# Kernel optimization log

Hardware: AMD Instinct MI355X
Metric: run time of the kernel (lower is better)

Reference implementation:

```python
import jax, jax.numpy as jnp
import numpy as np

N = 100000       # nodes
E = 1600000      # edges
V = 50000        # vocab
H = 256          # embedding dim (hsize)
A = 64           # per-head out dim (asize)
NH = 3           # num_heads
G = 64           # graphs in batch


def setup_inputs() -> dict:
    key = jax.random.key(0)
    ks = jax.random.split(key, 12)
    h0 = jax.random.randint(ks[0], (N,), 0, V)
    src = jax.random.randint(ks[1], (E,), 0, N)
    dst = jax.random.randint(ks[2], (E,), 0, N)
    graph_ids = jnp.sort(jax.random.randint(ks[3], (N,), 0, G))
    s = 0.05
    emb = jax.random.normal(ks[4], (V, H), jnp.float32) * s
    W_fc = jax.random.normal(ks[5], (H, NH * A), jnp.float32) * s   # GATConv fc
    attn_l = jax.random.normal(ks[6], (NH, A), jnp.float32) * s
    attn_r = jax.random.normal(ks[7], (NH, A), jnp.float32) * s
    bias_gat = jax.random.normal(ks[8], (NH, A), jnp.float32) * s
    W1 = jax.random.normal(ks[9], (A, 128), jnp.float32) * s
    b1 = jnp.zeros((128,), jnp.float32)
    W2 = jax.random.normal(ks[10], (128, 16), jnp.float32) * s
    b2 = jnp.zeros((16,), jnp.float32)
    return dict(h0=h0, src=src, dst=dst, graph_ids=graph_ids, emb=emb,
                W_fc=W_fc, attn_l=attn_l, attn_r=attn_r, bias_gat=bias_gat,
                W1=W1, b1=b1, W2=W2, b2=b2)


def reference(h0, src, dst, graph_ids, emb, W_fc, attn_l, attn_r, bias_gat,
              W1, b1, W2, b2):
    # embedding lookup
    h1 = emb[h0]                                            # [N, H]
    # GATConv: linear projection per head
    feat = (h1 @ W_fc).reshape(N, NH, A)                    # [N, NH, A]
    el = jnp.einsum('nha,ha->nh', feat, attn_l)             # [N, NH]
    er = jnp.einsum('nha,ha->nh', feat, attn_r)             # [N, NH]
    e = jax.nn.leaky_relu(el[src] + er[dst], 0.2)           # [E, NH]
    # segment softmax over incoming edges of each dst node
    m = jax.ops.segment_max(e, dst, num_segments=N)         # [N, NH]
    e_exp = jnp.exp(e - m[dst])                             # [E, NH]
    denom = jax.ops.segment_sum(e_exp, dst, num_segments=N) # [N, NH]
    alpha = e_exp / denom[dst]                              # [E, NH]
    # scatter-aggregate messages
    msg = alpha[:, :, None] * feat[src]                     # [E, NH, A]
    rst = jax.ops.segment_sum(msg, dst, num_segments=N)     # [N, NH, A]
    rst = rst + bias_gat[None]                              # GATConv bias
    # relu + mean over heads
    h2 = jnp.mean(jax.nn.relu(rst), axis=1)                 # [N, A]
    # MLP predictor: ReLU then Identity
    h3 = jax.nn.relu(h2 @ W1 + b1) @ W2 + b2                # [N, 16]
    # dgl.mean_nodes: per-graph mean readout
    sums = jax.ops.segment_sum(h3, graph_ids, num_segments=G)            # [G, 16]
    counts = jax.ops.segment_sum(jnp.ones((N,), h3.dtype), graph_ids, num_segments=G)
    return sums / jnp.maximum(counts, 1.0)[:, None]         # [G, 16]
```

## Files before the change

kernel.cpp:

```cpp
#include <hip/hip_runtime.h>
#include <hip/hip_bf16.h>

#define NNODES 100000
#define NEDGES 1600000
#define VOCAB 50000
#define HDIM 256
#define ADIM 64
#define NHEADS 3
#define FDIM 192
#define NGRAPH 64
#define NPART 64

#define CONV_ELEMS (HDIM * FDIM + 128 * 64 + 16 * 128)
#define CONV_BLOCKS ((CONV_ELEMS + 255) / 256)
#define HIST_BLOCKS ((NEDGES + 255) / 256)
#define PREP_BLOCKS 3
#define ELVR_BLOCKS ((VOCAB + 3) / 4)
#define PROJ_BLOCKS ((VOCAB + 63) / 64)
#define SCAT_BLOCKS ((NEDGES / 4 + 255) / 256)
#define NB ((NNODES + 1023) / 1024)

typedef __attribute__((ext_vector_type(8))) short bf16x8;
typedef __attribute__((ext_vector_type(4))) float f32x4;

__device__ __forceinline__ float bf2f(unsigned short u) {
  return __uint_as_float((unsigned int)u << 16);
}
__device__ __forceinline__ unsigned short f2bf(float f) {
  unsigned int u = __float_as_uint(f);
  u += 0x7FFFu + ((u >> 16) & 1u);
  return (unsigned short)(u >> 16);
}

__global__ __launch_bounds__(256) void conv_hist_prep_kernel(
    const float* __restrict__ Wfc, const float* __restrict__ W1,
    const float* __restrict__ W2, unsigned short* __restrict__ Wt,
    unsigned short* __restrict__ W1t, unsigned short* __restrict__ W2t,
    const int* __restrict__ src, const int* __restrict__ dst,
    const int* __restrict__ h0, int* __restrict__ cnt,
    unsigned short* __restrict__ rank16,
    unsigned short* __restrict__ vsrc16, unsigned short* __restrict__ vdst16,
    const float* __restrict__ al, const float* __restrict__ ar,
    float* __restrict__ wl, float* __restrict__ wr)
{
  if (blockIdx.x < CONV_BLOCKS) {
    int i = blockIdx.x * 256 + threadIdx.x;
    if (i < HDIM * FDIM) {
      int c = i / HDIM, k = i % HDIM;
      Wt[i] = f2bf(Wfc[(size_t)k * FDIM + c]);
    } else if (i < HDIM * FDIM + 128 * 64) {
      int j = i - HDIM * FDIM;
      int c = j / 64, k = j % 64;
      W1t[j] = f2bf(W1[(size_t)k * 128 + c]);
    } else if (i < CONV_ELEMS) {
      int j = i - HDIM * FDIM - 128 * 64;
      int c = j / 128, k = j % 128;
      W2t[j] = f2bf(W2[(size_t)k * 16 + c]);
    }
    return;
  }
  if (blockIdx.x < CONV_BLOCKS + HIST_BLOCKS) {
    int e = (blockIdx.x - CONV_BLOCKS) * 256 + threadIdx.x;
    if (e < NEDGES) {
      int s = src[e], d = dst[e];
      rank16[e]  = (unsigned short)atomicAdd(&cnt[d], 1);
      vsrc16[e]  = (unsigned short)h0[s];
      vdst16[e]  = (unsigned short)h0[d];
    }
    return;
  }
  int t = (blockIdx.x - CONV_BLOCKS - HIST_BLOCKS) * 256 + threadIdx.x;
  if (t >= 3 * 256) return;
  int h = t >> 8, k = t & 255;
  const float* a_l = &al[h * 64];
  const float* a_r = &ar[h * 64];
  const float* row = &Wfc[(size_t)k * FDIM + h * 64];
  float sl = 0.f, sr = 0.f;
#pragma unroll 16
  for (int c = 0; c < 64; ++c) {
    float w = row[c];
    sl += w * a_l[c];
    sr += w * a_r[c];
  }
  wl[h * 256 + k] = sl;
  wr[h * 256 + k] = sr;
}

__global__ __launch_bounds__(256) void scan_elvr_kernel(
    const int* __restrict__ cnt, int* __restrict__ offs,
    const float* __restrict__ emb, const float* __restrict__ wl,
    const float* __restrict__ wr, float4* __restrict__ elv4,
    float4* __restrict__ erv4)
{
  if (blockIdx.x < NB) {
    __shared__ int sd[256];
    __shared__ int base_sh;
    const int i = blockIdx.x, t = threadIdx.x;
    const int pre = i * 1024;
    int s = 0;
    for (int j = t * 4; j < pre; j += 1024) {
      int4 v = *reinterpret_cast<const int4*>(&cnt[j]);
      s += v.x + v.y + v.z + v.w;
    }
    sd[t] = s;
    __syncthreads();
    for (int o = 128; o > 0; o >>= 1) {
      if (t < o) sd[t] += sd[t + o];
      __syncthreads();
    }
    if (t == 0) base_sh = sd[0];
    __syncthreads();
    const int base = base_sh;
    __syncthreads();
    int bstart = pre + t * 4;
    int c[4];
    int ts = 0;
#pragma unroll
    for (int j = 0; j < 4; ++j) {
      c[j] = (bstart + j < NNODES) ? cnt[bstart + j] : 0;
      ts += c[j];
    }
    sd[t] = ts;
    __syncthreads();
    for (int o = 1; o < 256; o <<= 1) {
      int v = (t >= o) ? sd[t - o] : 0;
      __syncthreads();
      sd[t] += v;
      __syncthreads();
    }
    int run = sd[t] - ts + base;
#pragma unroll
    for (int j = 0; j < 4; ++j) {
      if (bstart + j < NNODES) offs[bstart + j] = run;
      run += c[j];
    }
    if (i == NB - 1 && t == 255) offs[NNODES] = base + sd[255];
    return;
  }
  int v = (blockIdx.x - NB) * 4 + (threadIdx.x >> 6);
  int lane = threadIdx.x & 63;
  if (v >= VOCAB) return;
  const float* er_ = &emb[(size_t)v * HDIM];
  float e0 = er_[lane], e1 = er_[64 + lane], e2 = er_[128 + lane], e3 = er_[192 + lane];
  float sl[3], sr[3];
#pragma unroll
  for (int h = 0; h < 3; ++h) {
    const float* wlh = &wl[h * 256];
    const float* wrh = &wr[h * 256];
    sl[h] = e0 * wlh[lane] + e1 * wlh[64 + lane] + e2 * wlh[128 + lane] + e3 * wlh[192 + lane];
    sr[h] = e0 * wrh[lane] + e1 * wrh[64 + lane] + e2 * wrh[128 + lane] + e3 * wrh[192 + lane];
  }
#pragma unroll
  for (int s = 32; s > 0; s >>= 1) {
#pragma unroll
    for (int h = 0; h < 3; ++h) {
      sl[h] += __shfl_xor(sl[h], s, 64);
      sr[h] += __shfl_xor(sr[h], s, 64);
    }
  }
  if (lane == 0) {
    elv4[v] = make_float4(sl[0], sl[1], sl[2], 0.f);
    erv4[v] = make_float4(sr[0], sr[1], sr[2], 0.f);
  }
}

__global__ __launch_bounds__(256) void proj_scatter_kernel(
    const float* __restrict__ emb,
    const unsigned short* __restrict__ Wt,
    unsigned short* __restrict__ proj_bf,
    const int* __restrict__ dst,
    const unsigned short* __restrict__ rank16,
    const unsigned short* __restrict__ vsrc16,
    const unsigned short* __restrict__ vdst16,
    const int* __restrict__ offs,
    const float4* __restrict__ elv4, const float4* __restrict__ erv4,
    uint2* __restrict__ wrec)
{
  if (blockIdx.x >= PROJ_BLOCKS) {
    int t = (blockIdx.x - PROJ_BLOCKS) * 256 + threadIdx.x;
    int e0 = t * 4;
    if (e0 >= NEDGES) return;
    int4    d4 = *reinterpret_cast<const int4*>(&dst[e0]);
    ushort4 r4 = *reinterpret_cast<const ushort4*>(&rank16[e0]);
    ushort4 s4 = *reinterpret_cast<const ushort4*>(&vsrc16[e0]);
    ushort4 v4 = *reinterpret_cast<const ushort4*>(&vdst16[e0]);
    int dd[4] = {d4.x, d4.y, d4.z, d4.w};
    int rr[4] = {r4.x, r4.y, r4.z, r4.w};
    int vs[4] = {s4.x, s4.y, s4.z, s4.w};
    int vd[4] = {v4.x, v4.y, v4.z, v4.w};
    float4 el[4], er[4];
    int of[4];
#pragma unroll
    for (int j = 0; j < 4; ++j) {
      el[j] = elv4[vs[j]];
      er[j] = erv4[vd[j]];
      of[j] = offs[dd[j]];
    }
#pragma unroll
    for (int j = 0; j < 4; ++j) {
      float e0f = el[j].x + er[j].x, e1f = el[j].y + er[j].y, e2f = el[j].z + er[j].z;
      e0f = e0f > 0.f ? e0f : 0.2f * e0f;
      e1f = e1f > 0.f ? e1f : 0.2f * e1f;
      e2f = e2f > 0.f ? e2f : 0.2f * e2f;
      unsigned short u0 = f2bf(__expf(e0f));
      unsigned short u1 = f2bf(__expf(e1f));
      unsigned short u2 = f2bf(__expf(e2f));
      wrec[of[j] + rr[j]] = make_uint2((unsigned)vs[j] | ((unsigned)u0 << 16),
                                       (unsigned)u1 | ((unsigned)u2 << 16));
    }
    return;
  }
  const int wave = threadIdx.x >> 6;
  const int lane = threadIdx.x & 63;
  const int row0 = blockIdx.x * 64 + wave * 16;
  const int cb = lane & 15;
  const int q  = lane >> 4;
  int arow = row0 + cb;
  if (arow >= VOCAB) arow = VOCAB - 1;
  const int kgrp = q * 8;

  f32x4 acc[12];
#pragma unroll
  for (int c = 0; c < 12; ++c) acc[c] = (f32x4){0.f, 0.f, 0.f, 0.f};

  const float* arow_p = &emb[(size_t)arow * HDIM + kgrp];
  const unsigned short* bcol_p = &Wt[(size_t)cb * HDIM + kgrp];

#pragma unroll
  for (int ks = 0; ks < 8; ++ks) {
    float4 f0 = *reinterpret_cast<const float4*>(arow_p + ks * 32);
    float4 f1 = *reinterpret_cast<const float4*>(arow_p + ks * 32 + 4);
    bf16x8 a;
    a[0] = (short)f2bf(f0.x); a[1] = (short)f2bf(f0.y);
    a[2] = (short)f2bf(f0.z); a[3] = (short)f2bf(f0.w);
    a[4] = (short)f2bf(f1.x); a[5] = (short)f2bf(f1.y);
    a[6] = (short)f2bf(f1.z); a[7] = (short)f2bf(f1.w);
#pragma unroll
    for (int c = 0; c < 12; ++c) {
      bf16x8 b = *reinterpret_cast<const bf16x8*>(bcol_p + (size_t)c * 16 * HDIM + ks * 32);
      acc[c] = __builtin_amdgcn_mfma_f32_16x16x32_bf16(a, b, acc[c], 0, 0, 0);
    }
  }

  const int rb = row0 + 4 * q;
#pragma unroll
  for (int i = 0; i < 4; ++i) {
    int r = rb + i;
    if (r < VOCAB) {
#pragma unroll
      for (int c = 0; c < 12; ++c)
        proj_bf[(size_t)r * FDIM + c * 16 + cb] = f2bf(acc[c][i]);
    }
  }
}

__global__ __launch_bounds__(256) void aggregate_kernel(
    const uint2* __restrict__ wrec, const int* __restrict__ offs,
    const unsigned short* __restrict__ proj_bf, const float* __restrict__ bias_gat,
    unsigned short* __restrict__ h2bf, int N)
{
  int lane = threadIdx.x & 63;
  int n = blockIdx.x * 4 + (threadIdx.x >> 6);
  if (n >= N) return;
  int lo = offs[n], hi = offs[n + 1];
  float a0 = 0.f, a1 = 0.f, a2 = 0.f, d0 = 0.f, d1 = 0.f, d2 = 0.f;

  int i = lo;
  for (; i + 4 <= hi; i += 4) {
    uint2 r[4];
#pragma unroll
    for (int j = 0; j < 4; ++j) r[j] = wrec[i + j];
    const unsigned short* ps[4];
#pragma unroll
    for (int j = 0; j < 4; ++j)
      ps[j] = &proj_bf[(size_t)(r[j].x & 0xFFFFu) * FDIM];
    float g0[4], g1[4], g2[4];
#pragma unroll
    for (int j = 0; j < 4; ++j) {
      g0[j] = bf2f(ps[j][lane]);
      g1[j] = bf2f(ps[j][64 + lane]);
      g2[j] = bf2f(ps[j][128 + lane]);
    }
#pragma unroll
    for (int j = 0; j < 4; ++j) {
      float w0 = bf2f((unsigned short)(r[j].x >> 16));
      float w1 = bf2f((unsigned short)(r[j].y & 0xFFFFu));
      float w2 = bf2f((unsigned short)(r[j].y >> 16));
      a0 += w0 * g0[j]; a1 += w1 * g1[j]; a2 += w2 * g2[j];
      d0 += w0; d1 += w1; d2 += w2;
    }
  }
  for (; i < hi; ++i) {
    uint2 r = wrec[i];
    const unsigned short* ps = &proj_bf[(size_t)(r.x & 0xFFFFu) * FDIM];
    float w0 = bf2f((unsigned short)(r.x >> 16));
    float w1 = bf2f((unsigned short)(r.y & 0xFFFFu));
    float w2 = bf2f((unsigned short)(r.y >> 16));
    a0 += w0 * bf2f(ps[lane]);
    a1 += w1 * bf2f(ps[64 + lane]);
    a2 += w2 * bf2f(ps[128 + lane]);
    d0 += w0; d1 += w1; d2 += w2;
  }

  float i0 = d0 > 0.f ? 1.f / d0 : 0.f;
  float i1 = d1 > 0.f ? 1.f / d1 : 0.f;
  float i2 = d2 > 0.f ? 1.f / d2 : 0.f;
  float r0 = a0 * i0 + bias_gat[lane];
  float r1 = a1 * i1 + bias_gat[64 + lane];
  float r2 = a2 * i2 + bias_gat[128 + lane];
  float h2 = (fmaxf(r0, 0.f) + fmaxf(r1, 0.f) + fmaxf(r2, 0.f)) * (1.f / 3.f);
  h2bf[(size_t)n * 64 + lane] = f2bf(h2);
}

__global__ __launch_bounds__(256) void post_mfma_kernel(
    const unsigned short* __restrict__ h2bf,
    const unsigned short* __restrict__ W1t,
    const float* __restrict__ b1,
    const unsigned short* __restrict__ W2t,
    const float* __restrict__ b2, const int* __restrict__ gid,
    float* __restrict__ sums_priv, float* __restrict__ counts_priv, int N)
{
  __shared__ unsigned short z_lds[64 * 128];
  const int wave = threadIdx.x >> 6;
  const int lane = threadIdx.x & 63;
  const int r = lane & 15;
  const int q = lane >> 4;
  const int kg = q * 8;
  const int rw0 = blockIdx.x * 64 + wave * 16;

  int arow = rw0 + r;
  if (arow >= N) arow = N - 1;

  f32x4 acc1[8];
#pragma unroll
  for (int c = 0; c < 8; ++c) acc1[c] = (f32x4){0.f, 0.f, 0.f, 0.f};

#pragma unroll
  for (int ks = 0; ks < 2; ++ks) {
    bf16x8 a = *reinterpret_cast<const bf16x8*>(&h2bf[(size_t)arow * 64 + kg + ks * 32]);
#pragma unroll
    for (int c = 0; c < 8; ++c) {
      bf16x8 b = *reinterpret_cast<const bf16x8*>(&W1t[(size_t)(c * 16 + r) * 64 + kg + ks * 32]);
      acc1[c] = __builtin_amdgcn_mfma_f32_16x16x32_bf16(a, b, acc1[c], 0, 0, 0);
    }
  }
#pragma unroll
  for (int c = 0; c < 8; ++c) {
    float bb = b1[c * 16 + r];
#pragma unroll
    for (int i = 0; i < 4; ++i) {
      float z = acc1[c][i] + bb;
      z = z > 0.f ? z : 0.f;
      z_lds[(wave * 16 + 4 * q + i) * 128 + c * 16 + r] = f2bf(z);
    }
  }
  __syncthreads();

  f32x4 acc2 = (f32x4){0.f, 0.f, 0.f, 0.f};
#pragma unroll
  for (int ks = 0; ks < 4; ++ks) {
    bf16x8 a = *reinterpret_cast<const bf16x8*>(&z_lds[(wave * 16 + r) * 128 + kg + ks * 32]);
    bf16x8 b = *reinterpret_cast<const bf16x8*>(&W2t[(size_t)r * 128 + kg + ks * 32]);
    acc2 = __builtin_amdgcn_mfma_f32_16x16x32_bf16(a, b, acc2, 0, 0, 0);
  }
  const int part = blockIdx.x & (NPART - 1);
  float bb2 = b2[r];
#pragma unroll
  for (int i = 0; i < 4; ++i) {
    int row = rw0 + 4 * q + i;
    if (row < N) {
      int g = gid[row];
      atomicAdd(&sums_priv[(part * NGRAPH + g) * 16 + r], acc2[i] + bb2);
      if (r == 0) atomicAdd(&counts_priv[part * NGRAPH + g], 1.f);
    }
  }
}

__global__ void finalize_kernel(const float* __restrict__ sums_priv,
                                const float* __restrict__ counts_priv,
                                float* __restrict__ out)
{
  int j = threadIdx.x;
  int g = j >> 4;
  float s = 0.f, c = 0.f;
  for (int p = 0; p < NPART; ++p) {
    s += sums_priv[p * NGRAPH * 16 + j];
    c += counts_priv[p * NGRAPH + g];
  }
  out[j] = s / fmaxf(c, 1.f);
}

extern "C" void kernel_launch(void* const* d_in, const int* in_sizes, int n_in,
                              void* d_out, int out_size, void* d_ws, size_t ws_size,
                              hipStream_t stream)
{
  const int*   h0  = (const int*)  d_in[0];
  const int*   src = (const int*)  d_in[1];
  const int*   dst = (const int*)  d_in[2];
  const int*   gid = (const int*)  d_in[3];
  const float* emb = (const float*)d_in[4];
  const float* Wfc = (const float*)d_in[5];
  const float* al  = (const float*)d_in[6];
  const float* ar  = (const float*)d_in[7];
  const float* bg  = (const float*)d_in[8];
  const float* W1  = (const float*)d_in[9];
  const float* b1  = (const float*)d_in[10];
  const float* W2  = (const float*)d_in[11];
  const float* b2  = (const float*)d_in[12];
  float* out = (float*)d_out;

  char* ws = (char*)d_ws;
  size_t off = 0;
  auto alloc = [&](size_t bytes) -> void* {
    off = (off + 255) & ~(size_t)255;
    void* p = ws + off;
    off += bytes;
    return p;
  };
  const size_t CNT_B  = (size_t)NNODES * 4;
  const size_t CNT_BP = (CNT_B + 255) & ~(size_t)255;
  const size_t SUMS_B = (size_t)NPART * NGRAPH * 16 * 4;
  const size_t ZB     = CNT_BP + SUMS_B + (size_t)NPART * NGRAPH * 4;
  char*  zero_base = (char*)alloc(ZB);
  int*   cnt  = (int*)zero_base;
  float* sums = (float*)(zero_base + CNT_BP);
  float* cnts = (float*)(zero_base + CNT_BP + SUMS_B);

  unsigned short* Wt      = (unsigned short*)alloc((size_t)FDIM * HDIM * 2);
  unsigned short* W1t     = (unsigned short*)alloc((size_t)128 * 64 * 2);
  unsigned short* W2t     = (unsigned short*)alloc((size_t)16 * 128 * 2);
  unsigned short* proj_bf = (unsigned short*)alloc((size_t)VOCAB * FDIM * 2);
  unsigned short* h2bf    = (unsigned short*)alloc((size_t)NNODES * 64 * 2);
  unsigned short* rank16  = (unsigned short*)alloc((size_t)NEDGES * 2);
  unsigned short* vsrc16  = (unsigned short*)alloc((size_t)NEDGES * 2);
  unsigned short* vdst16  = (unsigned short*)alloc((size_t)NEDGES * 2);
  uint2*  wrec   = (uint2*) alloc((size_t)NEDGES * 8);
  float4* elv4   = (float4*)alloc((size_t)VOCAB * 16);
  float4* erv4   = (float4*)alloc((size_t)VOCAB * 16);
  float*  wl     = (float*) alloc((size_t)3 * 256 * 4);
  float*  wr     = (float*) alloc((size_t)3 * 256 * 4);
  int*    offs   = (int*)   alloc((size_t)(NNODES + 1) * 4);

  hipMemsetAsync(zero_base, 0, ZB, stream);

  conv_hist_prep_kernel<<<CONV_BLOCKS + HIST_BLOCKS + PREP_BLOCKS, 256, 0, stream>>>(
      Wfc, W1, W2, Wt, W1t, W2t, src, dst, h0, cnt, rank16, vsrc16, vdst16,
      al, ar, wl, wr);
  scan_elvr_kernel<<<NB + ELVR_BLOCKS, 256, 0, stream>>>(
      cnt, offs, emb, wl, wr, elv4, erv4);
  proj_scatter_kernel<<<PROJ_BLOCKS + SCAT_BLOCKS, 256, 0, stream>>>(
      emb, Wt, proj_bf, dst, rank16, vsrc16, vdst16, offs, elv4, erv4, wrec);
  aggregate_kernel<<<(NNODES + 3) / 4, 256, 0, stream>>>(wrec, offs, proj_bf,
                                                         bg, h2bf, NNODES);
  post_mfma_kernel<<<(NNODES + 63) / 64, 256, 0, stream>>>(h2bf, W1t, b1, W2t, b2, gid,
                                                           sums, cnts, NNODES);
  finalize_kernel<<<1, 1024, 0, stream>>>(sums, cnts, out);
}
```

Before: 322.0 us.

## Vectorize aggregate gathers with 8-byte per-lane loads and unroll scatter to 8 edges

The aggregate kernel now maps lanes to (head, 4-column chunk), so each lane loads 8 bytes of a projected row instead of three 2-byte loads. It unrolls the edge loop to 8 edges and combines heads with cross-lane shuffles before writing. The scatter part of the projection kernel handles 8 edges per thread instead of 4, which halves its block count. The aim is fewer, wider memory transactions on the latency-bound gather. In exchange, lanes 48-63 duplicate head 2's work and only 16 lanes store results.

```diff
diff --git a/kernel.cpp b/kernel.cpp
--- a/kernel.cpp
+++ b/kernel.cpp
@@ -17,7 +17,7 @@
 #define PREP_BLOCKS 3
 #define ELVR_BLOCKS ((VOCAB + 3) / 4)
 #define PROJ_BLOCKS ((VOCAB + 63) / 64)
-#define SCAT_BLOCKS ((NEDGES / 4 + 255) / 256)
+#define SCAT_BLOCKS ((NEDGES / 8 + 255) / 256)
 #define NB ((NNODES + 1023) / 1024)
 
 typedef __attribute__((ext_vector_type(8))) short bf16x8;
@@ -178,26 +178,30 @@
 {
   if (blockIdx.x >= PROJ_BLOCKS) {
     int t = (blockIdx.x - PROJ_BLOCKS) * 256 + threadIdx.x;
-    int e0 = t * 4;
+    int e0 = t * 8;
     if (e0 >= NEDGES) return;
-    int4    d4 = *reinterpret_cast<const int4*>(&dst[e0]);
-    ushort4 r4 = *reinterpret_cast<const ushort4*>(&rank16[e0]);
-    ushort4 s4 = *reinterpret_cast<const ushort4*>(&vsrc16[e0]);
-    ushort4 v4 = *reinterpret_cast<const ushort4*>(&vdst16[e0]);
-    int dd[4] = {d4.x, d4.y, d4.z, d4.w};
-    int rr[4] = {r4.x, r4.y, r4.z, r4.w};
-    int vs[4] = {s4.x, s4.y, s4.z, s4.w};
-    int vd[4] = {v4.x, v4.y, v4.z, v4.w};
-    float4 el[4], er[4];
-    int of[4];
-#pragma unroll
-    for (int j = 0; j < 4; ++j) {
+    int4    dA = *reinterpret_cast<const int4*>(&dst[e0]);
+    int4    dB = *reinterpret_cast<const int4*>(&dst[e0 + 4]);
+    ushort4 rA = *reinterpret_cast<const ushort4*>(&rank16[e0]);
+    ushort4 rB = *reinterpret_cast<const ushort4*>(&rank16[e0 + 4]);
+    ushort4 sA = *reinterpret_cast<const ushort4*>(&vsrc16[e0]);
+    ushort4 sB = *reinterpret_cast<const ushort4*>(&vsrc16[e0 + 4]);
+    ushort4 vA = *reinterpret_cast<const ushort4*>(&vdst16[e0]);
+    ushort4 vB = *reinterpret_cast<const ushort4*>(&vdst16[e0 + 4]);
+    int dd[8] = {dA.x, dA.y, dA.z, dA.w, dB.x, dB.y, dB.z, dB.w};
+    int rr[8] = {rA.x, rA.y, rA.z, rA.w, rB.x, rB.y, rB.z, rB.w};
+    int vs[8] = {sA.x, sA.y, sA.z, sA.w, sB.x, sB.y, sB.z, sB.w};
+    int vd[8] = {vA.x, vA.y, vA.z, vA.w, vB.x, vB.y, vB.z, vB.w};
+    float4 el[8], er[8];
+    int of[8];
+#pragma unroll
+    for (int j = 0; j < 8; ++j) {
       el[j] = elv4[vs[j]];
       er[j] = erv4[vd[j]];
       of[j] = offs[dd[j]];
     }
 #pragma unroll
-    for (int j = 0; j < 4; ++j) {
+    for (int j = 0; j < 8; ++j) {
       float e0f = el[j].x + er[j].x, e1f = el[j].y + er[j].y, e2f = el[j].z + er[j].z;
       e0f = e0f > 0.f ? e0f : 0.2f * e0f;
       e1f = e1f > 0.f ? e1f : 0.2f * e1f;
@@ -259,57 +263,79 @@
     const unsigned short* __restrict__ proj_bf, const float* __restrict__ bias_gat,
     unsigned short* __restrict__ h2bf, int N)
 {
-  int lane = threadIdx.x & 63;
-  int n = blockIdx.x * 4 + (threadIdx.x >> 6);
+  const int lane = threadIdx.x & 63;
+  const int n = blockIdx.x * 4 + (threadIdx.x >> 6);
   if (n >= N) return;
+  int head = lane >> 4; if (head > 2) head = 2;
+  const int sub = lane & 15;
+  const char* pbase = (const char*)proj_bf;
+  const unsigned lane_off = (unsigned)(head * 128 + sub * 8);
+
   int lo = offs[n], hi = offs[n + 1];
-  float a0 = 0.f, a1 = 0.f, a2 = 0.f, d0 = 0.f, d1 = 0.f, d2 = 0.f;
+  float a0 = 0.f, a1 = 0.f, a2 = 0.f, a3 = 0.f, d = 0.f;
 
   int i = lo;
-  for (; i + 4 <= hi; i += 4) {
-    uint2 r[4];
-#pragma unroll
-    for (int j = 0; j < 4; ++j) r[j] = wrec[i + j];
-    const unsigned short* ps[4];
-#pragma unroll
-    for (int j = 0; j < 4; ++j)
-      ps[j] = &proj_bf[(size_t)(r[j].x & 0xFFFFu) * FDIM];
-    float g0[4], g1[4], g2[4];
-#pragma unroll
-    for (int j = 0; j < 4; ++j) {
-      g0[j] = bf2f(ps[j][lane]);
-      g1[j] = bf2f(ps[j][64 + lane]);
-      g2[j] = bf2f(ps[j][128 + lane]);
-    }
-#pragma unroll
-    for (int j = 0; j < 4; ++j) {
-      float w0 = bf2f((unsigned short)(r[j].x >> 16));
-      float w1 = bf2f((unsigned short)(r[j].y & 0xFFFFu));
-      float w2 = bf2f((unsigned short)(r[j].y >> 16));
-      a0 += w0 * g0[j]; a1 += w1 * g1[j]; a2 += w2 * g2[j];
-      d0 += w0; d1 += w1; d2 += w2;
+  for (; i + 8 <= hi; i += 8) {
+    uint2 r[8];
+#pragma unroll
+    for (int j = 0; j < 8; ++j) r[j] = wrec[i + j];
+    const char* pa[8];
+    float w[8];
+#pragma unroll
+    for (int j = 0; j < 8; ++j) {
+      unsigned v = r[j].x & 0xFFFFu;
+      pa[j] = pbase + (size_t)(v * 384u + lane_off);
+      unsigned wb = (head == 0) ? (r[j].x & 0xFFFF0000u)
+                  : (head == 1) ? (r[j].y << 16)
+                                : (r[j].y & 0xFFFF0000u);
+      w[j] = __uint_as_float(wb);
+    }
+    uint2 g[8];
+#pragma unroll
+    for (int j = 0; j < 8; ++j)
+      g[j] = *reinterpret_cast<const uint2*>(pa[j]);
+#pragma unroll
+    for (int j = 0; j < 8; ++j) {
+      a0 += w[j] * __uint_as_float(g[j].x << 16);
+      a1 += w[j] * __uint_as_float(g[j].x & 0xFFFF0000u);
+      a2 += w[j] * __uint_as_float(g[j].y << 16);
+      a3 += w[j] * __uint_as_float(g[j].y & 0xFFFF0000u);
+      d  += w[j];
     }
   }
   for (; i < hi; ++i) {
     uint2 r = wrec[i];
-    const unsigned short* ps = &proj_bf[(size_t)(r.x & 0xFFFFu) * FDIM];
-    float w0 = bf2f((unsigned short)(r.x >> 16));
-    float w1 = bf2f((unsigned short)(r.y & 0xFFFFu));
-    float w2 = bf2f((unsigned short)(r.y >> 16));
-    a0 += w0 * bf2f(ps[lane]);
-    a1 += w1 * bf2f(ps[64 + lane]);
-    a2 += w2 * bf2f(ps[128 + lane]);
-    d0 += w0; d1 += w1; d2 += w2;
-  }
-
-  float i0 = d0 > 0.f ? 1.f / d0 : 0.f;
-  float i1 = d1 > 0.f ? 1.f / d1 : 0.f;
-  float i2 = d2 > 0.f ? 1.f / d2 : 0.f;
-  float r0 = a0 * i0 + bias_gat[lane];
-  float r1 = a1 * i1 + bias_gat[64 + lane];
-  float r2 = a2 * i2 + bias_gat[128 + lane];
-  float h2 = (fmaxf(r0, 0.f) + fmaxf(r1, 0.f) + fmaxf(r2, 0.f)) * (1.f / 3.f);
-  h2bf[(size_t)n * 64 + lane] = f2bf(h2);
+    unsigned v = r.x & 0xFFFFu;
+    unsigned wb = (head == 0) ? (r.x & 0xFFFF0000u)
+                : (head == 1) ? (r.y << 16)
+                              : (r.y & 0xFFFF0000u);
+    float w = __uint_as_float(wb);
+    uint2 g = *reinterpret_cast<const uint2*>(pbase + (size_t)(v * 384u + lane_off));
+    a0 += w * __uint_as_float(g.x << 16);
+    a1 += w * __uint_as_float(g.x & 0xFFFF0000u);
+    a2 += w * __uint_as_float(g.y << 16);
+    a3 += w * __uint_as_float(g.y & 0xFFFF0000u);
+    d  += w;
+  }
+
+  float inv = d > 0.f ? 1.f / d : 0.f;
+  float4 bb = *reinterpret_cast<const float4*>(&bias_gat[head * 64 + sub * 4]);
+  float r0 = fmaxf(a0 * inv + bb.x, 0.f);
+  float r1 = fmaxf(a1 * inv + bb.y, 0.f);
+  float r2 = fmaxf(a2 * inv + bb.z, 0.f);
+  float r3 = fmaxf(a3 * inv + bb.w, 0.f);
+  float s0 = r0 + __shfl(r0, lane + 16, 64) + __shfl(r0, lane + 32, 64);
+  float s1 = r1 + __shfl(r1, lane + 16, 64) + __shfl(r1, lane + 32, 64);
+  float s2 = r2 + __shfl(r2, lane + 16, 64) + __shfl(r2, lane + 32, 64);
+  float s3 = r3 + __shfl(r3, lane + 16, 64) + __shfl(r3, lane + 32, 64);
+  if (lane < 16) {
+    ushort4 o;
+    o.x = f2bf(s0 * (1.f / 3.f));
+    o.y = f2bf(s1 * (1.f / 3.f));
+    o.z = f2bf(s2 * (1.f / 3.f));
+    o.w = f2bf(s3 * (1.f / 3.f));
+    *reinterpret_cast<ushort4*>(&h2bf[(size_t)n * 64 + sub * 4]) = o;
+  }
 }
 
 __global__ __launch_bounds__(256) void post_mfma_kernel(
```

Measured after the change: 338.3 us. 5.1% more time.
